# Optimization experiments

Hardware: AMD Instinct MI355X
Metric: run time of the kernel (lower is better)

Reference implementation:

```python
import jax, jax.numpy as jnp
import numpy as np

D_MODEL = 256
NUM_TYPES = 20
T_MAX = 200.0
LENGTH_SCALE = 1.0
ALPHA = 1.0
LN_EPS = 1e-6


def setup_inputs() -> dict:
    key = jax.random.key(0)
    kt, ktype, kat, kw, kwt, kbt = jax.random.split(key, 6)
    B, S = 4, 4096
    # event times: sorted uniform in [0, T_MAX] per sequence
    event_time = jnp.sort(jax.random.uniform(kt, (B, S), jnp.float32) * T_MAX, axis=-1)
    event_type = jax.random.randint(ktype, (B, S), 1, NUM_TYPES + 1, jnp.int32)
    arrival_times = jax.random.uniform(kat, (B, S), jnp.float32) * T_MAX
    # decoder params: input_weights (no bias), event_time_calculator (d->1, bias)
    W_in = jax.random.normal(kw, (D_MODEL, D_MODEL), jnp.float32) / np.sqrt(D_MODEL)
    w_t = jax.random.normal(kwt, (D_MODEL,), jnp.float32) / np.sqrt(D_MODEL)
    b_t = jax.random.normal(kbt, (), jnp.float32)
    ln_gamma = jnp.ones((D_MODEL,), jnp.float32)
    ln_beta = jnp.zeros((D_MODEL,), jnp.float32)
    return {"event_type": event_type, "event_time": event_time,
            "arrival_times": arrival_times, "W_in": W_in, "w_t": w_t,
            "b_t": b_t, "ln_gamma": ln_gamma, "ln_beta": ln_beta}


def reference(event_type, event_time, arrival_times, W_in, w_t, b_t, ln_gamma, ln_beta):
    B, S = event_time.shape
    # sinusoidal temporal encoding: w_k[i] = 10000^(2*(i//2+1)/d_model)
    i = jnp.arange(D_MODEL)
    w_k = jnp.power(10000.0, 2.0 * (i // 2 + 1).astype(jnp.float32) / D_MODEL)
    te = event_time[:, :, None] / w_k                       # [B,S,D]
    embedding = jnp.where(i % 2 == 0, jnp.sin(te), jnp.cos(te))
    # squared-exponential kernel on pairwise time differences, causal-masked
    dt = event_time[:, :, None] - event_time[:, None, :]    # [B,S,S]
    scores = ALPHA * jnp.exp(-(dt * dt) / (2.0 * LENGTH_SCALE ** 2))
    causal = jnp.tril(jnp.ones((S, S), bool))               # keep j <= i
    scores = jnp.where(causal, scores, 0.0)
    hidden = jnp.einsum('bij,bjd->bid', scores, embedding)  # [B,S,D]
    # LayerNorm (eps=1e-6)
    mu = hidden.mean(-1, keepdims=True)
    var = jnp.mean((hidden - mu) ** 2, axis=-1, keepdims=True)
    hidden = (hidden - mu) * jax.lax.rsqrt(var + LN_EPS) * ln_gamma + ln_beta
    # decoder: relu(linear) -> softplus(linear->1)
    hs = jax.nn.relu(jnp.einsum('bsd,ed->bse', hidden, W_in))
    out = jax.nn.softplus(jnp.einsum('bsd,d->bs', hs, w_t) + b_t)
    return out
```

## Files before the change

kernel.cpp:

```cpp
#include <hip/hip_runtime.h>
#include <hip/hip_bf16.h>
#include <math.h>

#define D 256
#define S 4096
#define BATCH 4
#define RPB 16
#define NBLK (BATCH * S / RPB)
#define DT_CUT 7.0f

typedef __attribute__((ext_vector_type(8))) short short8;
typedef __attribute__((ext_vector_type(4))) float f32x4;

static __device__ __forceinline__ unsigned short f2bf(float x) {
    union { __hip_bfloat16 b; unsigned short u; } cv;
    cv.b = __float2bfloat16(x);
    return cv.u;
}


__global__ __launch_bounds__(256) void prep_kernel(const float* __restrict__ t,
                                                   const float* __restrict__ W,
                                                   unsigned short* __restrict__ w5,
                                                   int* __restrict__ jcmin_out) {
    int blk = blockIdx.x;
    int tid = threadIdx.x;

    {
        int e = blk, dd = tid;
        int et16 = e >> 4, l15 = e & 15;
        int kt = dd >> 5, kgg = (dd >> 3) & 3, ee = dd & 7;
        w5[(size_t)((et16 * 8 + kt) * 512) + (kgg * 16 + l15) * 8 + ee]
            = f2bf(W[e * D + dd]);
    }

    if (tid < 64) {
#pragma unroll
        for (int s = 0; s < 4; ++s) {
            int fb = blk * 4 + s;
            int b2 = fb >> 8;
            int i0 = (fb & 255) * RPB;
            const float* tb2 = t + b2 * S;
            float tcut = tb2[i0] - DT_CUT;
            int lo = 0, hi = i0;
            while (hi > lo) {
                int step = ((hi - lo) + 63) >> 6;
                int p = min(lo + tid * step, hi);
                unsigned long long mb = __ballot(tb2[p] < tcut);
                int cnt = __popcll(mb);
                int nlo = (cnt == 0) ? lo : (lo + (cnt - 1) * step + 1);
                int nhi = (cnt == 0) ? nlo : min(lo + cnt * step, hi);
                lo = nlo; hi = nhi;
            }
            if (tid == 0) jcmin_out[fb] = lo >> 5;
        }
    }
}

__global__ __launch_bounds__(256, 4) void fused_kernel(
    const float* __restrict__ t, const unsigned short* __restrict__ w5,
    const int* __restrict__ jcmin_arr,
    const float* __restrict__ gamma, const float* __restrict__ beta,
    const float* __restrict__ w_t, const float* __restrict__ b_t,
    float* __restrict__ out) {
    int bid  = blockIdx.x;
    int blk  = (bid & 7) * (NBLK / 8) + (bid >> 3);
    int b    = blk >> 8;
    int i0   = (blk & 255) * RPB;
    int tid  = threadIdx.x;
    int w    = tid >> 6;
    int lane = tid & 63;
    int ln15 = lane & 15;
    int kg   = lane >> 4;
    const float* tb = t + b * S;

    float ti = tb[i0 + ln15];
    int   ir = i0 + ln15;
    int jcmin = jcmin_arr[blk];
    int jcmax = (i0 + RPB - 1) >> 5;

    const float c2 = -0.1038102552f;
    float cr[4];
#pragma unroll
    for (int nt = 0; nt < 4; ++nt) {
        int d = w * 64 + nt * 16 + ln15;
        cr[nt] = exp2f(c2 * (float)((d >> 1) + 1));
    }
    float phase = (ln15 & 1) ? 1.5707963268f : 0.0f;

    f32x4 acc[4];
#pragma unroll
    for (int nt = 0; nt < 4; ++nt) acc[nt] = (f32x4){0.f, 0.f, 0.f, 0.f};

    for (int jc = jcmin; jc <= jcmax; ++jc) {
        int j0 = jc * 32;
        float4 ta4 = *(const float4*)&tb[j0 + kg * 8];
        float4 tb4 = *(const float4*)&tb[j0 + kg * 8 + 4];
        float tj[8] = {ta4.x, ta4.y, ta4.z, ta4.w, tb4.x, tb4.y, tb4.z, tb4.w};

        union { short8 v; unsigned short u[8]; } a;
        if (jc < jcmax) {
#pragma unroll
            for (int e = 0; e < 8; ++e) {
                float d0 = ti - tj[e];
                a.u[e] = f2bf(__expf(-0.5f * d0 * d0));
            }
        } else {
#pragma unroll
            for (int e = 0; e < 8; ++e) {
                int j = j0 + kg * 8 + e;
                float d0 = ti - tj[e];
                float s0 = __expf(-0.5f * d0 * d0);
                a.u[e] = (j <= ir) ? f2bf(s0) : (unsigned short)0;
            }
        }
#pragma unroll
        for (int nt = 0; nt < 4; ++nt) {
            union { short8 v; unsigned short u[8]; } bf;
#pragma unroll
            for (int e = 0; e < 8; ++e)
                bf.u[e] = f2bf(__sinf(fmaf(tj[e], cr[nt], phase)));
            acc[nt] = __builtin_amdgcn_mfma_f32_16x16x32_bf16(a.v, bf.v, acc[nt], 0, 0, 0);
        }
    }

    const unsigned short* wbase = w5 + (size_t)(w * 4 * 8) * 512 + lane * 8;
    short8 w0 = *(const short8*)(wbase + (size_t)(0 * 8) * 512);
    short8 w1 = *(const short8*)(wbase + (size_t)(1 * 8) * 512);
    short8 w2 = *(const short8*)(wbase + (size_t)(2 * 8) * 512);
    short8 w3 = *(const short8*)(wbase + (size_t)(3 * 8) * 512);

    __shared__ float2 s_ln[4][RPB];
    __shared__ unsigned short H[RPB][264];
    __shared__ float s_dec[4][RPB];

#pragma unroll
    for (int reg = 0; reg < 4; ++reg) {
        float s = acc[0][reg] + acc[1][reg] + acc[2][reg] + acc[3][reg];
        float q = acc[0][reg] * acc[0][reg] + acc[1][reg] * acc[1][reg]
                + acc[2][reg] * acc[2][reg] + acc[3][reg] * acc[3][reg];
#pragma unroll
        for (int m = 1; m < 16; m <<= 1) {
            s += __shfl_xor(s, m);
            q += __shfl_xor(q, m);
        }
        if (ln15 == 0) s_ln[w][kg * 4 + reg] = make_float2(s, q);
    }
    __syncthreads();

    float g[4], be[4];
#pragma unroll
    for (int nt = 0; nt < 4; ++nt) {
        g[nt]  = gamma[w * 64 + nt * 16 + ln15];
        be[nt] = beta[w * 64 + nt * 16 + ln15];
    }
#pragma unroll
    for (int reg = 0; reg < 4; ++reg) {
        int r = kg * 4 + reg;
        float2 p0 = s_ln[0][r], p1 = s_ln[1][r], p2 = s_ln[2][r], p3 = s_ln[3][r];
        float sum = p0.x + p1.x + p2.x + p3.x;
        float sq  = p0.y + p1.y + p2.y + p3.y;
        float mu  = sum * (1.0f / D);
        float var = fmaxf(sq * (1.0f / D) - mu * mu, 0.0f);
        float rstd = rsqrtf(var + 1e-6f);
#pragma unroll
        for (int nt = 0; nt < 4; ++nt) {
            float h = (acc[nt][reg] - mu) * rstd * g[nt] + be[nt];
            H[r][w * 64 + nt * 16 + ln15] = f2bf(h);
        }
    }
    __syncthreads();

    f32x4 acc2[4];
#pragma unroll
    for (int et = 0; et < 4; ++et) acc2[et] = (f32x4){0.f, 0.f, 0.f, 0.f};

#pragma unroll
    for (int kt = 0; kt < 8; ++kt) {
        short8 nw0, nw1, nw2, nw3;
        if (kt < 7) {
            const unsigned short* p = wbase + (size_t)(kt + 1) * 512;
            nw0 = *(const short8*)(p + (size_t)(0 * 8) * 512);
            nw1 = *(const short8*)(p + (size_t)(1 * 8) * 512);
            nw2 = *(const short8*)(p + (size_t)(2 * 8) * 512);
            nw3 = *(const short8*)(p + (size_t)(3 * 8) * 512);
        }
        short8 a0 = *(const short8*)&H[ln15][kt * 32 + kg * 8];
        acc2[0] = __builtin_amdgcn_mfma_f32_16x16x32_bf16(a0, w0, acc2[0], 0, 0, 0);
        acc2[1] = __builtin_amdgcn_mfma_f32_16x16x32_bf16(a0, w1, acc2[1], 0, 0, 0);
        acc2[2] = __builtin_amdgcn_mfma_f32_16x16x32_bf16(a0, w2, acc2[2], 0, 0, 0);
        acc2[3] = __builtin_amdgcn_mfma_f32_16x16x32_bf16(a0, w3, acc2[3], 0, 0, 0);
        w0 = nw0; w1 = nw1; w2 = nw2; w3 = nw3;
    }

    float wt[4];
#pragma unroll
    for (int et = 0; et < 4; ++et) wt[et] = w_t[w * 64 + et * 16 + ln15];
#pragma unroll
    for (int reg = 0; reg < 4; ++reg) {
        float v = 0.f;
#pragma unroll
        for (int et = 0; et < 4; ++et)
            v = fmaf(fmaxf(acc2[et][reg], 0.f), wt[et], v);
#pragma unroll
        for (int m = 1; m < 16; m <<= 1) v += __shfl_xor(v, m);
        if (ln15 == 0) s_dec[w][kg * 4 + reg] = v;
    }
    __syncthreads();
    if (tid < RPB) {
        float tot = s_dec[0][tid] + s_dec[1][tid] + s_dec[2][tid] + s_dec[3][tid] + b_t[0];
        float o = fmaxf(tot, 0.0f) + log1pf(expf(-fabsf(tot)));
        out[(size_t)blk * RPB + tid] = o;
    }
}

extern "C" void kernel_launch(void* const* d_in, const int* in_sizes, int n_in,
                              void* d_out, int out_size, void* d_ws, size_t ws_size,
                              hipStream_t stream) {
    const float* t   = (const float*)d_in[1];
    const float* W   = (const float*)d_in[3];
    const float* wt  = (const float*)d_in[4];
    const float* bt  = (const float*)d_in[5];
    const float* gam = (const float*)d_in[6];
    const float* bet = (const float*)d_in[7];
    float* out = (float*)d_out;

    char* ws = (char*)d_ws;
    unsigned short* w5    = (unsigned short*)ws;
    int*            jcmin = (int*)(ws + (size_t)131072);

    prep_kernel<<<dim3(256), dim3(256), 0, stream>>>(t, W, w5, jcmin);
    fused_kernel<<<dim3(NBLK), dim3(256), 0, stream>>>(
        t, w5, jcmin, gam, bet, wt, bt, out);
}
```

Baseline: 27.27 us.

## Process 32 rows per block, reusing sinusoid B-fragments across two M tiles

Doubles rows per block from 16 to 32 so each sinusoidal embedding fragment, which costs a sin per element, feeds two MFMA row tiles instead of one. This halves redundant sin/bf16 conversion work and W fragment loads per row, and halves the grid size. In exchange it raises register pressure (launch bounds drop to 2 blocks per CU), gives fewer blocks for load balance, and per-block loops are slightly longer because the j-range covers more rows.

```diff
diff --git a/kernel.cpp b/kernel.cpp
--- a/kernel.cpp
+++ b/kernel.cpp
@@ -5,7 +5,7 @@
 #define D 256
 #define S 4096
 #define BATCH 4
-#define RPB 16
+#define RPB 32
 #define NBLK (BATCH * S / RPB)
 #define DT_CUT 7.0f
 
@@ -36,10 +36,10 @@
 
     if (tid < 64) {
 #pragma unroll
-        for (int s = 0; s < 4; ++s) {
-            int fb = blk * 4 + s;
-            int b2 = fb >> 8;
-            int i0 = (fb & 255) * RPB;
+        for (int s = 0; s < 2; ++s) {
+            int fb = blk * 2 + s;
+            int b2 = fb >> 7;
+            int i0 = (fb & 127) * RPB;
             const float* tb2 = t + b2 * S;
             float tcut = tb2[i0] - DT_CUT;
             int lo = 0, hi = i0;
@@ -57,7 +57,7 @@
     }
 }
 
-__global__ __launch_bounds__(256, 4) void fused_kernel(
+__global__ __launch_bounds__(256, 2) void fused_kernel(
     const float* __restrict__ t, const unsigned short* __restrict__ w5,
     const int* __restrict__ jcmin_arr,
     const float* __restrict__ gamma, const float* __restrict__ beta,
@@ -65,8 +65,8 @@
     float* __restrict__ out) {
     int bid  = blockIdx.x;
     int blk  = (bid & 7) * (NBLK / 8) + (bid >> 3);
-    int b    = blk >> 8;
-    int i0   = (blk & 255) * RPB;
+    int b    = blk >> 7;
+    int i0   = (blk & 127) * RPB;
     int tid  = threadIdx.x;
     int w    = tid >> 6;
     int lane = tid & 63;
@@ -74,10 +74,10 @@
     int kg   = lane >> 4;
     const float* tb = t + b * S;
 
-    float ti = tb[i0 + ln15];
-    int   ir = i0 + ln15;
+    float ti0 = tb[i0 + ln15], ti1 = tb[i0 + 16 + ln15];
+    int   ir0 = i0 + ln15,     ir1 = i0 + 16 + ln15;
     int jcmin = jcmin_arr[blk];
-    int jcmax = (i0 + RPB - 1) >> 5;
+    int jcmax = i0 >> 5;
 
     const float c2 = -0.1038102552f;
     float cr[4];
@@ -88,31 +88,24 @@
     }
     float phase = (ln15 & 1) ? 1.5707963268f : 0.0f;
 
-    f32x4 acc[4];
-#pragma unroll
-    for (int nt = 0; nt < 4; ++nt) acc[nt] = (f32x4){0.f, 0.f, 0.f, 0.f};
-
-    for (int jc = jcmin; jc <= jcmax; ++jc) {
+    f32x4 acc[2][4];
+#pragma unroll
+    for (int Mt = 0; Mt < 2; ++Mt)
+#pragma unroll
+        for (int nt = 0; nt < 4; ++nt) acc[Mt][nt] = (f32x4){0.f, 0.f, 0.f, 0.f};
+
+    for (int jc = jcmin; jc < jcmax; ++jc) {
         int j0 = jc * 32;
         float4 ta4 = *(const float4*)&tb[j0 + kg * 8];
         float4 tb4 = *(const float4*)&tb[j0 + kg * 8 + 4];
         float tj[8] = {ta4.x, ta4.y, ta4.z, ta4.w, tb4.x, tb4.y, tb4.z, tb4.w};
 
-        union { short8 v; unsigned short u[8]; } a;
-        if (jc < jcmax) {
-#pragma unroll
-            for (int e = 0; e < 8; ++e) {
-                float d0 = ti - tj[e];
-                a.u[e] = f2bf(__expf(-0.5f * d0 * d0));
-            }
-        } else {
-#pragma unroll
-            for (int e = 0; e < 8; ++e) {
-                int j = j0 + kg * 8 + e;
-                float d0 = ti - tj[e];
-                float s0 = __expf(-0.5f * d0 * d0);
-                a.u[e] = (j <= ir) ? f2bf(s0) : (unsigned short)0;
-            }
+        union { short8 v; unsigned short u[8]; } a0, a1;
+#pragma unroll
+        for (int e = 0; e < 8; ++e) {
+            float d0 = ti0 - tj[e], d1 = ti1 - tj[e];
+            a0.u[e] = f2bf(__expf(-0.5f * d0 * d0));
+            a1.u[e] = f2bf(__expf(-0.5f * d1 * d1));
         }
 #pragma unroll
         for (int nt = 0; nt < 4; ++nt) {
@@ -120,7 +113,33 @@
 #pragma unroll
             for (int e = 0; e < 8; ++e)
                 bf.u[e] = f2bf(__sinf(fmaf(tj[e], cr[nt], phase)));
-            acc[nt] = __builtin_amdgcn_mfma_f32_16x16x32_bf16(a.v, bf.v, acc[nt], 0, 0, 0);
+            acc[0][nt] = __builtin_amdgcn_mfma_f32_16x16x32_bf16(a0.v, bf.v, acc[0][nt], 0, 0, 0);
+            acc[1][nt] = __builtin_amdgcn_mfma_f32_16x16x32_bf16(a1.v, bf.v, acc[1][nt], 0, 0, 0);
+        }
+    }
+    {
+        int j0 = jcmax * 32;
+        float4 ta4 = *(const float4*)&tb[j0 + kg * 8];
+        float4 tb4 = *(const float4*)&tb[j0 + kg * 8 + 4];
+        float tj[8] = {ta4.x, ta4.y, ta4.z, ta4.w, tb4.x, tb4.y, tb4.z, tb4.w};
+
+        union { short8 v; unsigned short u[8]; } a0, a1;
+#pragma unroll
+        for (int e = 0; e < 8; ++e) {
+            int j = j0 + kg * 8 + e;
+            float d0 = ti0 - tj[e], d1 = ti1 - tj[e];
+            float s0 = __expf(-0.5f * d0 * d0), s1 = __expf(-0.5f * d1 * d1);
+            a0.u[e] = (j <= ir0) ? f2bf(s0) : (unsigned short)0;
+            a1.u[e] = (j <= ir1) ? f2bf(s1) : (unsigned short)0;
+        }
+#pragma unroll
+        for (int nt = 0; nt < 4; ++nt) {
+            union { short8 v; unsigned short u[8]; } bf;
+#pragma unroll
+            for (int e = 0; e < 8; ++e)
+                bf.u[e] = f2bf(__sinf(fmaf(tj[e], cr[nt], phase)));
+            acc[0][nt] = __builtin_amdgcn_mfma_f32_16x16x32_bf16(a0.v, bf.v, acc[0][nt], 0, 0, 0);
+            acc[1][nt] = __builtin_amdgcn_mfma_f32_16x16x32_bf16(a1.v, bf.v, acc[1][nt], 0, 0, 0);
         }
     }
 
@@ -135,17 +154,19 @@
     __shared__ float s_dec[4][RPB];
 
 #pragma unroll
-    for (int reg = 0; reg < 4; ++reg) {
-        float s = acc[0][reg] + acc[1][reg] + acc[2][reg] + acc[3][reg];
-        float q = acc[0][reg] * acc[0][reg] + acc[1][reg] * acc[1][reg]
-                + acc[2][reg] * acc[2][reg] + acc[3][reg] * acc[3][reg];
-#pragma unroll
-        for (int m = 1; m < 16; m <<= 1) {
-            s += __shfl_xor(s, m);
-            q += __shfl_xor(q, m);
-        }
-        if (ln15 == 0) s_ln[w][kg * 4 + reg] = make_float2(s, q);
-    }
+    for (int Mt = 0; Mt < 2; ++Mt)
+#pragma unroll
+        for (int reg = 0; reg < 4; ++reg) {
+            float s = acc[Mt][0][reg] + acc[Mt][1][reg] + acc[Mt][2][reg] + acc[Mt][3][reg];
+            float q = acc[Mt][0][reg] * acc[Mt][0][reg] + acc[Mt][1][reg] * acc[Mt][1][reg]
+                    + acc[Mt][2][reg] * acc[Mt][2][reg] + acc[Mt][3][reg] * acc[Mt][3][reg];
+#pragma unroll
+            for (int m = 1; m < 16; m <<= 1) {
+                s += __shfl_xor(s, m);
+                q += __shfl_xor(q, m);
+            }
+            if (ln15 == 0) s_ln[w][Mt * 16 + kg * 4 + reg] = make_float2(s, q);
+        }
     __syncthreads();
 
     float g[4], be[4];
@@ -155,25 +176,29 @@
         be[nt] = beta[w * 64 + nt * 16 + ln15];
     }
 #pragma unroll
-    for (int reg = 0; reg < 4; ++reg) {
-        int r = kg * 4 + reg;
-        float2 p0 = s_ln[0][r], p1 = s_ln[1][r], p2 = s_ln[2][r], p3 = s_ln[3][r];
-        float sum = p0.x + p1.x + p2.x + p3.x;
-        float sq  = p0.y + p1.y + p2.y + p3.y;
-        float mu  = sum * (1.0f / D);
-        float var = fmaxf(sq * (1.0f / D) - mu * mu, 0.0f);
-        float rstd = rsqrtf(var + 1e-6f);
-#pragma unroll
-        for (int nt = 0; nt < 4; ++nt) {
-            float h = (acc[nt][reg] - mu) * rstd * g[nt] + be[nt];
-            H[r][w * 64 + nt * 16 + ln15] = f2bf(h);
-        }
-    }
+    for (int Mt = 0; Mt < 2; ++Mt)
+#pragma unroll
+        for (int reg = 0; reg < 4; ++reg) {
+            int r = Mt * 16 + kg * 4 + reg;
+            float2 p0 = s_ln[0][r], p1 = s_ln[1][r], p2 = s_ln[2][r], p3 = s_ln[3][r];
+            float sum = p0.x + p1.x + p2.x + p3.x;
+            float sq  = p0.y + p1.y + p2.y + p3.y;
+            float mu  = sum * (1.0f / D);
+            float var = fmaxf(sq * (1.0f / D) - mu * mu, 0.0f);
+            float rstd = rsqrtf(var + 1e-6f);
+#pragma unroll
+            for (int nt = 0; nt < 4; ++nt) {
+                float h = (acc[Mt][nt][reg] - mu) * rstd * g[nt] + be[nt];
+                H[r][w * 64 + nt * 16 + ln15] = f2bf(h);
+            }
+        }
     __syncthreads();
 
-    f32x4 acc2[4];
-#pragma unroll
-    for (int et = 0; et < 4; ++et) acc2[et] = (f32x4){0.f, 0.f, 0.f, 0.f};
+    f32x4 acc2[2][4];
+#pragma unroll
+    for (int Mt = 0; Mt < 2; ++Mt)
+#pragma unroll
+        for (int et = 0; et < 4; ++et) acc2[Mt][et] = (f32x4){0.f, 0.f, 0.f, 0.f};
 
 #pragma unroll
     for (int kt = 0; kt < 8; ++kt) {
@@ -186,10 +211,15 @@
             nw3 = *(const short8*)(p + (size_t)(3 * 8) * 512);
         }
         short8 a0 = *(const short8*)&H[ln15][kt * 32 + kg * 8];
-        acc2[0] = __builtin_amdgcn_mfma_f32_16x16x32_bf16(a0, w0, acc2[0], 0, 0, 0);
-        acc2[1] = __builtin_amdgcn_mfma_f32_16x16x32_bf16(a0, w1, acc2[1], 0, 0, 0);
-        acc2[2] = __builtin_amdgcn_mfma_f32_16x16x32_bf16(a0, w2, acc2[2], 0, 0, 0);
-        acc2[3] = __builtin_amdgcn_mfma_f32_16x16x32_bf16(a0, w3, acc2[3], 0, 0, 0);
+        short8 a1 = *(const short8*)&H[16 + ln15][kt * 32 + kg * 8];
+        acc2[0][0] = __builtin_amdgcn_mfma_f32_16x16x32_bf16(a0, w0, acc2[0][0], 0, 0, 0);
+        acc2[0][1] = __builtin_amdgcn_mfma_f32_16x16x32_bf16(a0, w1, acc2[0][1], 0, 0, 0);
+        acc2[0][2] = __builtin_amdgcn_mfma_f32_16x16x32_bf16(a0, w2, acc2[0][2], 0, 0, 0);
+        acc2[0][3] = __builtin_amdgcn_mfma_f32_16x16x32_bf16(a0, w3, acc2[0][3], 0, 0, 0);
+        acc2[1][0] = __builtin_amdgcn_mfma_f32_16x16x32_bf16(a1, w0, acc2[1][0], 0, 0, 0);
+        acc2[1][1] = __builtin_amdgcn_mfma_f32_16x16x32_bf16(a1, w1, acc2[1][1], 0, 0, 0);
+        acc2[1][2] = __builtin_amdgcn_mfma_f32_16x16x32_bf16(a1, w2, acc2[1][2], 0, 0, 0);
+        acc2[1][3] = __builtin_amdgcn_mfma_f32_16x16x32_bf16(a1, w3, acc2[1][3], 0, 0, 0);
         w0 = nw0; w1 = nw1; w2 = nw2; w3 = nw3;
     }
 
@@ -197,15 +227,17 @@
 #pragma unroll
     for (int et = 0; et < 4; ++et) wt[et] = w_t[w * 64 + et * 16 + ln15];
 #pragma unroll
-    for (int reg = 0; reg < 4; ++reg) {
-        float v = 0.f;
-#pragma unroll
-        for (int et = 0; et < 4; ++et)
-            v = fmaf(fmaxf(acc2[et][reg], 0.f), wt[et], v);
-#pragma unroll
-        for (int m = 1; m < 16; m <<= 1) v += __shfl_xor(v, m);
-        if (ln15 == 0) s_dec[w][kg * 4 + reg] = v;
-    }
+    for (int Mt = 0; Mt < 2; ++Mt)
+#pragma unroll
+        for (int reg = 0; reg < 4; ++reg) {
+            float v = 0.f;
+#pragma unroll
+            for (int et = 0; et < 4; ++et)
+                v = fmaf(fmaxf(acc2[Mt][et][reg], 0.f), wt[et], v);
+#pragma unroll
+            for (int m = 1; m < 16; m <<= 1) v += __shfl_xor(v, m);
+            if (ln15 == 0) s_dec[w][Mt * 16 + kg * 4 + reg] = v;
+        }
     __syncthreads();
     if (tid < RPB) {
         float tot = s_dec[0][tid] + s_dec[1][tid] + s_dec[2][tid] + s_dec[3][tid] + b_t[0];
```

New measurement: 24.72 us. -9.3%, faster.

## Enlarge row tile to 64 with shared-memory operand generation and reuse

Applied to the files above, without the earlier changes.

Each block now handles 64 query rows with 512 threads instead of 16 rows with 256. Kernel weights and sinusoid embedding tiles are generated once per 32-column chunk into double-buffered shared memory and reused across four row sub-tiles, and sin and cos are produced together with sincos. The aim is to cut the redundant transcendental work in the old layout, where each block recomputed embeddings for only 16 rows, and to amortize W loads in the decoder GEMM. In exchange, the grid shrinks to 256 blocks, which may underfill the GPU, and each block adds per-chunk barriers and processes a wider causal window.

```diff
diff --git a/kernel.cpp b/kernel.cpp
--- a/kernel.cpp
+++ b/kernel.cpp
@@ -5,7 +5,7 @@
 #define D 256
 #define S 4096
 #define BATCH 4
-#define RPB 16
+#define RPB 64
 #define NBLK (BATCH * S / RPB)
 #define DT_CUT 7.0f
 
@@ -35,29 +35,25 @@
     }
 
     if (tid < 64) {
-#pragma unroll
-        for (int s = 0; s < 4; ++s) {
-            int fb = blk * 4 + s;
-            int b2 = fb >> 8;
-            int i0 = (fb & 255) * RPB;
-            const float* tb2 = t + b2 * S;
-            float tcut = tb2[i0] - DT_CUT;
-            int lo = 0, hi = i0;
-            while (hi > lo) {
-                int step = ((hi - lo) + 63) >> 6;
-                int p = min(lo + tid * step, hi);
-                unsigned long long mb = __ballot(tb2[p] < tcut);
-                int cnt = __popcll(mb);
-                int nlo = (cnt == 0) ? lo : (lo + (cnt - 1) * step + 1);
-                int nhi = (cnt == 0) ? nlo : min(lo + cnt * step, hi);
-                lo = nlo; hi = nhi;
-            }
-            if (tid == 0) jcmin_out[fb] = lo >> 5;
-        }
-    }
-}
-
-__global__ __launch_bounds__(256, 4) void fused_kernel(
+        int b2 = blk >> 6;
+        int i0 = (blk & 63) * RPB;
+        const float* tb2 = t + b2 * S;
+        float tcut = tb2[i0] - DT_CUT;
+        int lo = 0, hi = i0;
+        while (hi > lo) {
+            int step = ((hi - lo) + 63) >> 6;
+            int p = min(lo + tid * step, hi);
+            unsigned long long mb = __ballot(tb2[p] < tcut);
+            int cnt = __popcll(mb);
+            int nlo = (cnt == 0) ? lo : (lo + (cnt - 1) * step + 1);
+            int nhi = (cnt == 0) ? nlo : min(lo + cnt * step, hi);
+            lo = nlo; hi = nhi;
+        }
+        if (tid == 0) jcmin_out[blk] = lo >> 5;
+    }
+}
+
+__global__ __launch_bounds__(512) void fused_kernel(
     const float* __restrict__ t, const unsigned short* __restrict__ w5,
     const int* __restrict__ jcmin_arr,
     const float* __restrict__ gamma, const float* __restrict__ beta,
@@ -65,8 +61,8 @@
     float* __restrict__ out) {
     int bid  = blockIdx.x;
     int blk  = (bid & 7) * (NBLK / 8) + (bid >> 3);
-    int b    = blk >> 8;
-    int i0   = (blk & 255) * RPB;
+    int b    = blk >> 6;
+    int i0   = (blk & 63) * RPB;
     int tid  = threadIdx.x;
     int w    = tid >> 6;
     int lane = tid & 63;
@@ -74,141 +70,171 @@
     int kg   = lane >> 4;
     const float* tb = t + b * S;
 
-    float ti = tb[i0 + ln15];
-    int   ir = i0 + ln15;
     int jcmin = jcmin_arr[blk];
     int jcmax = (i0 + RPB - 1) >> 5;
 
+    __shared__ unsigned short Ag[2][2048];
+    __shared__ unsigned short Bg[2][8192];
+    __shared__ unsigned short H[RPB][264];
+    __shared__ float2 s_ln[8][RPB];
+    __shared__ float  s_mu[RPB], s_rs[RPB];
+    __shared__ float  s_dec[8][RPB];
+
+    int mtA  = tid >> 7;
+    int lA   = (tid >> 1) & 63;
+    int hA   = (tid & 1) * 4;
+    int rowA = i0 + mtA * 16 + (lA & 15);
+    float tiA = tb[rowA];
+    int joffA = ((lA >> 4) << 3) + hA;
+    int aidx  = mtA * 512 + lA * 8 + hA;
     const float c2 = -0.1038102552f;
-    float cr[4];
-#pragma unroll
-    for (int nt = 0; nt < 4; ++nt) {
-        int d = w * 64 + nt * 16 + ln15;
-        cr[nt] = exp2f(c2 * (float)((d >> 1) + 1));
-    }
-    float phase = (ln15 & 1) ? 1.5707963268f : 0.0f;
-
-    f32x4 acc[4];
-#pragma unroll
-    for (int nt = 0; nt < 4; ++nt) acc[nt] = (f32x4){0.f, 0.f, 0.f, 0.f};
-
+    int ntB  = tid >> 5;
+    int lB   = (tid * 2) & 63;
+    int dB   = ntB * 16 + (lB & 15);
+    float crB = exp2f(c2 * (float)((dB >> 1) + 1));
+    int joffB = (lB >> 4) << 3;
+    int bidx0 = ntB * 512 + lB * 8;
+
+    auto gen = [&](int buf, int j0) {
+        float4 t4 = *(const float4*)&tb[j0 + joffA];
+        unsigned short a4[4];
+#pragma unroll
+        for (int c = 0; c < 4; ++c) {
+            float dd = tiA - ((const float*)&t4)[c];
+            float s = __expf(-0.5f * dd * dd);
+            a4[c] = (j0 + joffA + c <= rowA) ? f2bf(s) : (unsigned short)0;
+        }
+        unsigned long long apk = (unsigned long long)a4[0] |
+            ((unsigned long long)a4[1] << 16) | ((unsigned long long)a4[2] << 32) |
+            ((unsigned long long)a4[3] << 48);
+        *(unsigned long long*)&Ag[buf][aidx] = apk;
+        float4 u4 = *(const float4*)&tb[j0 + joffB];
+        float4 v4 = *(const float4*)&tb[j0 + joffB + 4];
+        float tjv[8] = {u4.x, u4.y, u4.z, u4.w, v4.x, v4.y, v4.z, v4.w};
+        union { short8 v; unsigned short u[8]; } b0, b1;
+#pragma unroll
+        for (int e = 0; e < 8; ++e) {
+            float sn, cs;
+            __sincosf(tjv[e] * crB, &sn, &cs);
+            b0.u[e] = f2bf(sn);
+            b1.u[e] = f2bf(cs);
+        }
+        *(short8*)&Bg[buf][bidx0]     = b0.v;
+        *(short8*)&Bg[buf][bidx0 + 8] = b1.v;
+    };
+
+    f32x4 acc[4][2];
+#pragma unroll
+    for (int mt = 0; mt < 4; ++mt)
+#pragma unroll
+        for (int sub = 0; sub < 2; ++sub) acc[mt][sub] = (f32x4){0.f, 0.f, 0.f, 0.f};
+
+    gen(0, jcmin * 32);
     for (int jc = jcmin; jc <= jcmax; ++jc) {
-        int j0 = jc * 32;
-        float4 ta4 = *(const float4*)&tb[j0 + kg * 8];
-        float4 tb4 = *(const float4*)&tb[j0 + kg * 8 + 4];
-        float tj[8] = {ta4.x, ta4.y, ta4.z, ta4.w, tb4.x, tb4.y, tb4.z, tb4.w};
-
-        union { short8 v; unsigned short u[8]; } a;
-        if (jc < jcmax) {
-#pragma unroll
-            for (int e = 0; e < 8; ++e) {
-                float d0 = ti - tj[e];
-                a.u[e] = f2bf(__expf(-0.5f * d0 * d0));
+        __syncthreads();
+        int buf = (jc - jcmin) & 1;
+        if (jc < jcmax) gen(buf ^ 1, (jc + 1) * 32);
+        short8 afr[4];
+#pragma unroll
+        for (int mt = 0; mt < 4; ++mt)
+            afr[mt] = *(const short8*)&Ag[buf][mt * 512 + lane * 8];
+        short8 bf0 = *(const short8*)&Bg[buf][(w * 2) * 512 + lane * 8];
+        short8 bf1 = *(const short8*)&Bg[buf][(w * 2 + 1) * 512 + lane * 8];
+#pragma unroll
+        for (int mt = 0; mt < 4; ++mt) {
+            acc[mt][0] = __builtin_amdgcn_mfma_f32_16x16x32_bf16(afr[mt], bf0, acc[mt][0], 0, 0, 0);
+            acc[mt][1] = __builtin_amdgcn_mfma_f32_16x16x32_bf16(afr[mt], bf1, acc[mt][1], 0, 0, 0);
+        }
+    }
+
+#pragma unroll
+    for (int mt = 0; mt < 4; ++mt)
+#pragma unroll
+        for (int reg = 0; reg < 4; ++reg) {
+            float v0 = acc[mt][0][reg], v1 = acc[mt][1][reg];
+            float s = v0 + v1;
+            float q = v0 * v0 + v1 * v1;
+#pragma unroll
+            for (int m = 1; m < 16; m <<= 1) {
+                s += __shfl_xor(s, m);
+                q += __shfl_xor(q, m);
             }
-        } else {
-#pragma unroll
-            for (int e = 0; e < 8; ++e) {
-                int j = j0 + kg * 8 + e;
-                float d0 = ti - tj[e];
-                float s0 = __expf(-0.5f * d0 * d0);
-                a.u[e] = (j <= ir) ? f2bf(s0) : (unsigned short)0;
-            }
-        }
-#pragma unroll
-        for (int nt = 0; nt < 4; ++nt) {
-            union { short8 v; unsigned short u[8]; } bf;
-#pragma unroll
-            for (int e = 0; e < 8; ++e)
-                bf.u[e] = f2bf(__sinf(fmaf(tj[e], cr[nt], phase)));
-            acc[nt] = __builtin_amdgcn_mfma_f32_16x16x32_bf16(a.v, bf.v, acc[nt], 0, 0, 0);
-        }
-    }
-
-    const unsigned short* wbase = w5 + (size_t)(w * 4 * 8) * 512 + lane * 8;
-    short8 w0 = *(const short8*)(wbase + (size_t)(0 * 8) * 512);
-    short8 w1 = *(const short8*)(wbase + (size_t)(1 * 8) * 512);
-    short8 w2 = *(const short8*)(wbase + (size_t)(2 * 8) * 512);
-    short8 w3 = *(const short8*)(wbase + (size_t)(3 * 8) * 512);
-
-    __shared__ float2 s_ln[4][RPB];
-    __shared__ unsigned short H[RPB][264];
-    __shared__ float s_dec[4][RPB];
-
-#pragma unroll
-    for (int reg = 0; reg < 4; ++reg) {
-        float s = acc[0][reg] + acc[1][reg] + acc[2][reg] + acc[3][reg];
-        float q = acc[0][reg] * acc[0][reg] + acc[1][reg] * acc[1][reg]
-                + acc[2][reg] * acc[2][reg] + acc[3][reg] * acc[3][reg];
-#pragma unroll
-        for (int m = 1; m < 16; m <<= 1) {
-            s += __shfl_xor(s, m);
-            q += __shfl_xor(q, m);
-        }
-        if (ln15 == 0) s_ln[w][kg * 4 + reg] = make_float2(s, q);
-    }
-    __syncthreads();
-
-    float g[4], be[4];
-#pragma unroll
-    for (int nt = 0; nt < 4; ++nt) {
-        g[nt]  = gamma[w * 64 + nt * 16 + ln15];
-        be[nt] = beta[w * 64 + nt * 16 + ln15];
-    }
-#pragma unroll
-    for (int reg = 0; reg < 4; ++reg) {
-        int r = kg * 4 + reg;
-        float2 p0 = s_ln[0][r], p1 = s_ln[1][r], p2 = s_ln[2][r], p3 = s_ln[3][r];
-        float sum = p0.x + p1.x + p2.x + p3.x;
-        float sq  = p0.y + p1.y + p2.y + p3.y;
+            if (ln15 == 0) s_ln[w][mt * 16 + kg * 4 + reg] = make_float2(s, q);
+        }
+    __syncthreads();
+    if (tid < RPB) {
+        float sum = 0.f, sq = 0.f;
+#pragma unroll
+        for (int ww = 0; ww < 8; ++ww) {
+            float2 p = s_ln[ww][tid];
+            sum += p.x; sq += p.y;
+        }
         float mu  = sum * (1.0f / D);
         float var = fmaxf(sq * (1.0f / D) - mu * mu, 0.0f);
-        float rstd = rsqrtf(var + 1e-6f);
-#pragma unroll
-        for (int nt = 0; nt < 4; ++nt) {
-            float h = (acc[nt][reg] - mu) * rstd * g[nt] + be[nt];
-            H[r][w * 64 + nt * 16 + ln15] = f2bf(h);
-        }
-    }
-    __syncthreads();
-
-    f32x4 acc2[4];
-#pragma unroll
-    for (int et = 0; et < 4; ++et) acc2[et] = (f32x4){0.f, 0.f, 0.f, 0.f};
+        s_mu[tid] = mu;
+        s_rs[tid] = rsqrtf(var + 1e-6f);
+    }
+    __syncthreads();
+
+    float g0 = gamma[w * 32 + ln15],      g1 = gamma[w * 32 + 16 + ln15];
+    float be0 = beta[w * 32 + ln15],      be1 = beta[w * 32 + 16 + ln15];
+#pragma unroll
+    for (int mt = 0; mt < 4; ++mt)
+#pragma unroll
+        for (int reg = 0; reg < 4; ++reg) {
+            int r = mt * 16 + kg * 4 + reg;
+            float mu = s_mu[r], rstd = s_rs[r];
+            H[r][w * 32 + ln15]      = f2bf((acc[mt][0][reg] - mu) * rstd * g0 + be0);
+            H[r][w * 32 + 16 + ln15] = f2bf((acc[mt][1][reg] - mu) * rstd * g1 + be1);
+        }
+    __syncthreads();
+
+    const unsigned short* wb0 = w5 + (size_t)((w * 2 + 0) * 8) * 512 + lane * 8;
+    const unsigned short* wb1 = w5 + (size_t)((w * 2 + 1) * 8) * 512 + lane * 8;
+    short8 W0 = *(const short8*)wb0;
+    short8 W1 = *(const short8*)wb1;
+
+    f32x4 acc2[4][2];
+#pragma unroll
+    for (int mt = 0; mt < 4; ++mt)
+#pragma unroll
+        for (int sub = 0; sub < 2; ++sub) acc2[mt][sub] = (f32x4){0.f, 0.f, 0.f, 0.f};
 
 #pragma unroll
     for (int kt = 0; kt < 8; ++kt) {
-        short8 nw0, nw1, nw2, nw3;
+        short8 nW0, nW1;
         if (kt < 7) {
-            const unsigned short* p = wbase + (size_t)(kt + 1) * 512;
-            nw0 = *(const short8*)(p + (size_t)(0 * 8) * 512);
-            nw1 = *(const short8*)(p + (size_t)(1 * 8) * 512);
-            nw2 = *(const short8*)(p + (size_t)(2 * 8) * 512);
-            nw3 = *(const short8*)(p + (size_t)(3 * 8) * 512);
-        }
-        short8 a0 = *(const short8*)&H[ln15][kt * 32 + kg * 8];
-        acc2[0] = __builtin_amdgcn_mfma_f32_16x16x32_bf16(a0, w0, acc2[0], 0, 0, 0);
-        acc2[1] = __builtin_amdgcn_mfma_f32_16x16x32_bf16(a0, w1, acc2[1], 0, 0, 0);
-        acc2[2] = __builtin_amdgcn_mfma_f32_16x16x32_bf16(a0, w2, acc2[2], 0, 0, 0);
-        acc2[3] = __builtin_amdgcn_mfma_f32_16x16x32_bf16(a0, w3, acc2[3], 0, 0, 0);
-        w0 = nw0; w1 = nw1; w2 = nw2; w3 = nw3;
-    }
-
-    float wt[4];
-#pragma unroll
-    for (int et = 0; et < 4; ++et) wt[et] = w_t[w * 64 + et * 16 + ln15];
-#pragma unroll
-    for (int reg = 0; reg < 4; ++reg) {
-        float v = 0.f;
-#pragma unroll
-        for (int et = 0; et < 4; ++et)
-            v = fmaf(fmaxf(acc2[et][reg], 0.f), wt[et], v);
-#pragma unroll
-        for (int m = 1; m < 16; m <<= 1) v += __shfl_xor(v, m);
-        if (ln15 == 0) s_dec[w][kg * 4 + reg] = v;
-    }
+            nW0 = *(const short8*)(wb0 + (size_t)(kt + 1) * 512);
+            nW1 = *(const short8*)(wb1 + (size_t)(kt + 1) * 512);
+        }
+        short8 a[4];
+#pragma unroll
+        for (int mt = 0; mt < 4; ++mt)
+            a[mt] = *(const short8*)&H[mt * 16 + ln15][kt * 32 + kg * 8];
+#pragma unroll
+        for (int mt = 0; mt < 4; ++mt) {
+            acc2[mt][0] = __builtin_amdgcn_mfma_f32_16x16x32_bf16(a[mt], W0, acc2[mt][0], 0, 0, 0);
+            acc2[mt][1] = __builtin_amdgcn_mfma_f32_16x16x32_bf16(a[mt], W1, acc2[mt][1], 0, 0, 0);
+        }
+        W0 = nW0; W1 = nW1;
+    }
+
+    float wt0 = w_t[w * 32 + ln15], wt1 = w_t[w * 32 + 16 + ln15];
+#pragma unroll
+    for (int mt = 0; mt < 4; ++mt)
+#pragma unroll
+        for (int reg = 0; reg < 4; ++reg) {
+            float v = fmaf(fmaxf(acc2[mt][0][reg], 0.f), wt0,
+                           fmaxf(acc2[mt][1][reg], 0.f) * wt1);
+#pragma unroll
+            for (int m = 1; m < 16; m <<= 1) v += __shfl_xor(v, m);
+            if (ln15 == 0) s_dec[w][mt * 16 + kg * 4 + reg] = v;
+        }
     __syncthreads();
     if (tid < RPB) {
-        float tot = s_dec[0][tid] + s_dec[1][tid] + s_dec[2][tid] + s_dec[3][tid] + b_t[0];
+        float tot = b_t[0];
+#pragma unroll
+        for (int ww = 0; ww < 8; ++ww) tot += s_dec[ww][tid];
         float o = fmaxf(tot, 0.0f) + log1pf(expf(-fabsf(tot)));
         out[(size_t)blk * RPB + tid] = o;
     }
@@ -230,6 +256,6 @@
     int*            jcmin = (int*)(ws + (size_t)131072);
 
     prep_kernel<<<dim3(256), dim3(256), 0, stream>>>(t, W, w5, jcmin);
-    fused_kernel<<<dim3(NBLK), dim3(256), 0, stream>>>(
+    fused_kernel<<<dim3(NBLK), dim3(512), 0, stream>>>(
         t, w5, jcmin, gam, bet, wt, bt, out);
 }
```

Result: faster. 25.43 us (-6.7%).
